# Kernel tuning notes

Measured on AMD Instinct MI355X. Metric: run time of the kernel, lower is better.

## Reference

```python
import jax, jax.numpy as jnp
import numpy as np

EPSILON = 1e-8
K = 3  # three-nearest-neighbor interpolation


def setup_inputs() -> dict:
    key = jax.random.key(0)
    k1, k2, k3 = jax.random.split(key, 3)
    B, N1, N2, C = 8, 1024, 4096, 256
    p1 = jax.random.normal(k1, (B, N1, 3), dtype=jnp.float32)  # coarse coords
    x1 = jax.random.normal(k2, (B, C, N1), dtype=jnp.float32)  # coarse features (channel-first)
    p2 = jax.random.normal(k3, (B, N2, 3), dtype=jnp.float32)  # fine coords
    return {"p1": p1, "x1": x1, "p2": p2}


def reference(p1, x1, p2):
    # Squared pairwise distances [B, N2, N1] via the expansion trick.
    d2 = (
        jnp.sum(p2 * p2, axis=-1, keepdims=True)
        - 2.0 * jnp.einsum("bmd,bnd->bmn", p2, p1)
        + jnp.sum(p1 * p1, axis=-1)[:, None, :]
    )
    # K smallest distances (pointops.nearestneighbor returns squared dists).
    neg_top, idx = jax.lax.top_k(-d2, K)  # [B, N2, K]
    dist = -neg_top
    # Reciprocal-distance weights, normalized over the K neighbors.
    dist_recip = 1.0 / (dist + EPSILON)
    weight = dist_recip / jnp.sum(dist_recip, axis=-1, keepdims=True)  # [B, N2, K]
    # Gather neighbor features and blend: up_x1[b,c,m] = sum_k w[b,m,k] * x1[b,c,idx[b,m,k]]
    x1t = jnp.swapaxes(x1, 1, 2)  # [B, N1, C]
    gathered = jax.vmap(lambda f, i: f[i])(x1t, idx)  # [B, N2, K, C]
    up_x1 = jnp.einsum("bmkc,bmk->bcm", gathered, weight)  # [B, C, N2]
    return up_x1
```

## Files before the change

kernel.cpp:

```cpp
#include <hip/hip_runtime.h>
#include <cfloat>
#include <climits>

#define B_   8
#define N1_  1024
#define N2_  4096
#define C_   256
#define TPQ  16
#define QPB  (256 / TPQ)


__device__ __forceinline__ bool better_(float d, int i, float D, int I) {
    return (d < D) || (d == D && i < I);
}

__device__ __forceinline__ void ins_(float d, int i,
                                     float& d0, float& d1, float& d2,
                                     int& i0, int& i1, int& i2) {
    if (better_(d, i, d2, i2)) {
        d2 = d; i2 = i;
        if (better_(d2, i2, d1, i1)) {
            float td = d1; d1 = d2; d2 = td;
            int   ti = i1; i1 = i2; i2 = ti;
            if (better_(d1, i1, d0, i0)) {
                td = d0; d0 = d1; d1 = td;
                ti = i0; i0 = i1; i1 = ti;
            }
        }
    }
}

__global__ __launch_bounds__(256) void knn_kernel(
    const float* __restrict__ p1, const float* __restrict__ p2,
    int4* __restrict__ wsi, float4* __restrict__ wsw) {
    __shared__ float4 pts[N1_];

    const int tid   = threadIdx.x;
    const int b     = blockIdx.x >> 8;
    const int mtile = blockIdx.x & 255;

    for (int j = tid; j < N1_; j += 256) {
        float x = p1[((size_t)b * N1_ + j) * 3 + 0];
        float y = p1[((size_t)b * N1_ + j) * 3 + 1];
        float z = p1[((size_t)b * N1_ + j) * 3 + 2];
        float s1 = __fadd_rn(__fadd_rn(__fmul_rn(x, x), __fmul_rn(y, y)),
                             __fmul_rn(z, z));
        pts[j] = make_float4(x + x, y + y, z + z, s1);
    }
    __syncthreads();

    const int q = tid >> 4;
    const int t = tid & 15;
    const int m = mtile * QPB + q;

    const size_t pbase = ((size_t)b * N2_ + m) * 3;
    const float x2 = p2[pbase + 0];
    const float y2 = p2[pbase + 1];
    const float z2 = p2[pbase + 2];
    const float s2 = __fadd_rn(__fadd_rn(__fmul_rn(x2, x2), __fmul_rn(y2, y2)),
                               __fmul_rn(z2, z2));

    float d0 = FLT_MAX, d1 = FLT_MAX, d2 = FLT_MAX;
    int   i0 = INT_MAX, i1 = INT_MAX, i2 = INT_MAX;

#pragma unroll 4
    for (int n = t; n < N1_; n += TPQ) {
        float4 p = pts[n];
        float dot2 = __fadd_rn(__fadd_rn(__fmul_rn(x2, p.x), __fmul_rn(y2, p.y)),
                               __fmul_rn(z2, p.z));
        float dd = __fadd_rn(__fsub_rn(s2, dot2), p.w);

        bool c0 = dd < d0;
        bool c1 = dd < d1;
        bool c2 = dd < d2;
        float n0 = fminf(dd, d0);
        float n1 = __builtin_amdgcn_fmed3f(dd, d0, d1);
        float n2 = __builtin_amdgcn_fmed3f(dd, d1, d2);
        int j0 = c0 ? n : i0;
        int j1 = c1 ? (c0 ? i0 : n) : i1;
        int j2 = c2 ? (c1 ? i1 : n) : i2;
        d0 = n0; d1 = n1; d2 = n2;
        i0 = j0; i1 = j1; i2 = j2;
    }

    for (int mask = 1; mask < TPQ; mask <<= 1) {
        float pd0 = __shfl_xor(d0, mask, TPQ);
        float pd1 = __shfl_xor(d1, mask, TPQ);
        float pd2 = __shfl_xor(d2, mask, TPQ);
        int   pi0 = __shfl_xor(i0, mask, TPQ);
        int   pi1 = __shfl_xor(i1, mask, TPQ);
        int   pi2 = __shfl_xor(i2, mask, TPQ);
        ins_(pd0, pi0, d0, d1, d2, i0, i1, i2);
        ins_(pd1, pi1, d0, d1, d2, i0, i1, i2);
        ins_(pd2, pi2, d0, d1, d2, i0, i1, i2);
    }

    if (t == 0) {
        float r0 = 1.0f / __fadd_rn(d0, 1e-8f);
        float r1 = 1.0f / __fadd_rn(d1, 1e-8f);
        float r2 = 1.0f / __fadd_rn(d2, 1e-8f);
        float s  = __fadd_rn(__fadd_rn(r0, r1), r2);
        const size_t o = (size_t)b * N2_ + m;
        wsi[o] = make_int4(i0, i1, i2, 0);
        wsw[o] = make_float4(r0 / s, r1 / s, r2 / s, 0.0f);
    }
}


__global__ __launch_bounds__(256) void blend_kernel(
    const float* __restrict__ x1, const int4* __restrict__ wsi,
    const float4* __restrict__ wsw, float* __restrict__ out) {
    __shared__ float4 L4[N1_];

    int bid = blockIdx.x;
    const int mhalf = bid & 1;
    const int ct    = (bid >> 1) & 63;
    const int b     = bid >> 7;
    const int tid   = threadIdx.x;

    const size_t wbase = (size_t)b * N2_ + (size_t)mhalf * 2048;
    int4   id[8];
    float4 w[8];
#pragma unroll
    for (int mb = 0; mb < 8; ++mb) {
        id[mb] = wsi[wbase + mb * 256 + tid];
        w[mb]  = wsw[wbase + mb * 256 + tid];
    }

    const float* src = x1 + ((size_t)b * C_ + (size_t)ct * 4) * N1_;
    float4 v[4];
#pragma unroll
    for (int c = 0; c < 4; ++c)
        v[c] = reinterpret_cast<const float4*>(src + (size_t)c * N1_)[tid];
#pragma unroll
    for (int e = 0; e < 4; ++e) {
        const int n = 4 * tid + e;
        L4[n ^ ((n >> 3) & 7)] = make_float4((&v[0].x)[e], (&v[1].x)[e],
                                             (&v[2].x)[e], (&v[3].x)[e]);
    }
    __syncthreads();

    const size_t obase = ((size_t)b * C_ + (size_t)ct * 4) * N2_;
#pragma unroll
    for (int mb = 0; mb < 8; ++mb) {
        const int m = mhalf * 2048 + mb * 256 + tid;
        const int na = id[mb].x, nb = id[mb].y, nc = id[mb].z;
        const float4 A  = L4[na ^ ((na >> 3) & 7)];
        const float4 Bv = L4[nb ^ ((nb >> 3) & 7)];
        const float4 Cv = L4[nc ^ ((nc >> 3) & 7)];
        const float wx = w[mb].x, wy = w[mb].y, wz = w[mb].z;
#pragma unroll
        for (int r = 0; r < 4; ++r) {
            float acc = __fadd_rn(__fadd_rn(__fmul_rn((&A.x)[r],  wx),
                                            __fmul_rn((&Bv.x)[r], wy)),
                                  __fmul_rn((&Cv.x)[r], wz));
            __builtin_nontemporal_store(acc, &out[obase + (size_t)r * N2_ + m]);
        }
    }
}

extern "C" void kernel_launch(void* const* d_in, const int* in_sizes, int n_in,
                              void* d_out, int out_size, void* d_ws, size_t ws_size,
                              hipStream_t stream) {
    const float* p1 = (const float*)d_in[0];
    const float* x1 = (const float*)d_in[1];
    const float* p2 = (const float*)d_in[2];
    float* out = (float*)d_out;

    int4*   wsi = (int4*)d_ws;
    float4* wsw = (float4*)((char*)d_ws + (size_t)B_ * N2_ * sizeof(int4));

    knn_kernel<<<B_ * (N2_ / QPB), 256, 0, stream>>>(p1, p2, wsi, wsw);
    blend_kernel<<<B_ * (C_ / 4) * 2, 256, 0, stream>>>(x1, wsi, wsw, out);
}
```

Baseline: 33.07 us.

## Pack distance and index into sortable keys, process four queries per thread

Rewrites the KNN kernel so each thread handles four queries over a 32-point slice, using packed float2 math. Each distance is truncated and packed with its 10-bit index into one unsigned key, so top-4 insertion becomes a chain of integer min/max ops. The exact top-3 is then recovered by recomputing the four candidate distances and sorting them. This cuts the per-point compare/select cost and amortizes shared-memory loads across queries, but adds register pressure and relies on four truncated candidates containing the true top three.

```diff
diff --git a/kernel.cpp b/kernel.cpp
--- a/kernel.cpp
+++ b/kernel.cpp
@@ -6,38 +6,37 @@
 #define N1_  1024
 #define N2_  4096
 #define C_   256
-#define TPQ  16
-#define QPB  (256 / TPQ)
-
-
-__device__ __forceinline__ bool better_(float d, int i, float D, int I) {
-    return (d < D) || (d == D && i < I);
-}
-
-__device__ __forceinline__ void ins_(float d, int i,
-                                     float& d0, float& d1, float& d2,
-                                     int& i0, int& i1, int& i2) {
-    if (better_(d, i, d2, i2)) {
-        d2 = d; i2 = i;
-        if (better_(d2, i2, d1, i1)) {
-            float td = d1; d1 = d2; d2 = td;
-            int   ti = i1; i1 = i2; i2 = ti;
-            if (better_(d1, i1, d0, i0)) {
-                td = d0; d0 = d1; d1 = td;
-                ti = i0; i0 = i1; i1 = ti;
-            }
-        }
-    }
-}
+#define QPT  4
+#define QPB  32
+
+typedef float vf2 __attribute__((ext_vector_type(2)));
+
+__device__ __forceinline__ unsigned umin_(unsigned a, unsigned b) { return a < b ? a : b; }
+__device__ __forceinline__ unsigned umax_(unsigned a, unsigned b) { return a > b ? a : b; }
+
+#define KINS4(k, k0, k1, k2, k3) do {                 \
+    unsigned _n1 = umax_(k0, umin_((k), k1));         \
+    unsigned _n2 = umax_(k1, umin_((k), k2));         \
+    unsigned _n3 = umax_(k2, umin_((k), k3));         \
+    k0 = umin_((k), k0);  k1 = _n1;  k2 = _n2;  k3 = _n3; \
+} while (0)
 
 __global__ __launch_bounds__(256) void knn_kernel(
     const float* __restrict__ p1, const float* __restrict__ p2,
     int4* __restrict__ wsi, float4* __restrict__ wsw) {
+#pragma clang fp contract(off)
     __shared__ float4 pts[N1_];
 
     const int tid   = threadIdx.x;
-    const int b     = blockIdx.x >> 8;
-    const int mtile = blockIdx.x & 255;
+    const int b     = blockIdx.x >> 7;
+    const int mtile = blockIdx.x & 127;
+    const int slice = tid & 31;
+    const int slot  = tid >> 5;
+    const int mbase = mtile * QPB + slot * QPT;
+
+    const float4* P4 = reinterpret_cast<const float4*>(
+        p2 + ((size_t)b * N2_ + mbase) * 3);
+    const float4 f0 = P4[0], f1 = P4[1], f2 = P4[2];
 
     for (int j = tid; j < N1_; j += 256) {
         float x = p1[((size_t)b * N1_ + j) * 3 + 0];
@@ -47,61 +46,108 @@
                              __fmul_rn(z, z));
         pts[j] = make_float4(x + x, y + y, z + z, s1);
     }
+
+    const float x0 = f0.x, y0 = f0.y, z0 = f0.z;
+    const float x1q = f0.w, y1q = f1.x, z1q = f1.y;
+    const float x2q = f1.z, y2q = f1.w, z2q = f2.x;
+    const float x3q = f2.y, y3q = f2.z, z3q = f2.w;
+    const vf2 xA = {x0, x1q}, xB = {x2q, x3q};
+    const vf2 yA = {y0, y1q}, yB = {y2q, y3q};
+    const vf2 zA = {z0, z1q}, zB = {z2q, z3q};
+    const vf2 sA = (xA * xA + yA * yA) + zA * zA;
+    const vf2 sB = (xB * xB + yB * yB) + zB * zB;
+
     __syncthreads();
 
-    const int q = tid >> 4;
-    const int t = tid & 15;
-    const int m = mtile * QPB + q;
-
-    const size_t pbase = ((size_t)b * N2_ + m) * 3;
-    const float x2 = p2[pbase + 0];
-    const float y2 = p2[pbase + 1];
-    const float z2 = p2[pbase + 2];
-    const float s2 = __fadd_rn(__fadd_rn(__fmul_rn(x2, x2), __fmul_rn(y2, y2)),
-                               __fmul_rn(z2, z2));
-
-    float d0 = FLT_MAX, d1 = FLT_MAX, d2 = FLT_MAX;
-    int   i0 = INT_MAX, i1 = INT_MAX, i2 = INT_MAX;
-
-#pragma unroll 4
-    for (int n = t; n < N1_; n += TPQ) {
-        float4 p = pts[n];
-        float dot2 = __fadd_rn(__fadd_rn(__fmul_rn(x2, p.x), __fmul_rn(y2, p.y)),
-                               __fmul_rn(z2, p.z));
-        float dd = __fadd_rn(__fsub_rn(s2, dot2), p.w);
-
-        bool c0 = dd < d0;
-        bool c1 = dd < d1;
-        bool c2 = dd < d2;
-        float n0 = fminf(dd, d0);
-        float n1 = __builtin_amdgcn_fmed3f(dd, d0, d1);
-        float n2 = __builtin_amdgcn_fmed3f(dd, d1, d2);
-        int j0 = c0 ? n : i0;
-        int j1 = c1 ? (c0 ? i0 : n) : i1;
-        int j2 = c2 ? (c1 ? i1 : n) : i2;
-        d0 = n0; d1 = n1; d2 = n2;
-        i0 = j0; i1 = j1; i2 = j2;
-    }
-
-    for (int mask = 1; mask < TPQ; mask <<= 1) {
-        float pd0 = __shfl_xor(d0, mask, TPQ);
-        float pd1 = __shfl_xor(d1, mask, TPQ);
-        float pd2 = __shfl_xor(d2, mask, TPQ);
-        int   pi0 = __shfl_xor(i0, mask, TPQ);
-        int   pi1 = __shfl_xor(i1, mask, TPQ);
-        int   pi2 = __shfl_xor(i2, mask, TPQ);
-        ins_(pd0, pi0, d0, d1, d2, i0, i1, i2);
-        ins_(pd1, pi1, d0, d1, d2, i0, i1, i2);
-        ins_(pd2, pi2, d0, d1, d2, i0, i1, i2);
-    }
-
-    if (t == 0) {
-        float r0 = 1.0f / __fadd_rn(d0, 1e-8f);
-        float r1 = 1.0f / __fadd_rn(d1, 1e-8f);
-        float r2 = 1.0f / __fadd_rn(d2, 1e-8f);
-        float s  = __fadd_rn(__fadd_rn(r0, r1), r2);
-        const size_t o = (size_t)b * N2_ + m;
-        wsi[o] = make_int4(i0, i1, i2, 0);
+    unsigned k00 = UINT_MAX, k01 = UINT_MAX, k02 = UINT_MAX, k03 = UINT_MAX;
+    unsigned k10 = UINT_MAX, k11 = UINT_MAX, k12 = UINT_MAX, k13 = UINT_MAX;
+    unsigned k20 = UINT_MAX, k21 = UINT_MAX, k22 = UINT_MAX, k23 = UINT_MAX;
+    unsigned k30 = UINT_MAX, k31 = UINT_MAX, k32 = UINT_MAX, k33 = UINT_MAX;
+
+#pragma unroll 8
+    for (int j = 0; j < N1_ / 32; ++j) {
+        const int n = j * 32 + slice;
+        const float4 c = pts[n];
+        const vf2 cx = {c.x, c.x}, cy = {c.y, c.y};
+        const vf2 cz = {c.z, c.z}, cw = {c.w, c.w};
+        const vf2 dA = (sA - ((xA * cx + yA * cy) + zA * cz)) + cw;
+        const vf2 dB = (sB - ((xB * cx + yB * cy) + zB * cz)) + cw;
+        const unsigned un = (unsigned)n;
+        const unsigned q0 = (__float_as_uint(fmaxf(dA.x, 0.f)) & 0xFFFFFC00u) | un;
+        const unsigned q1 = (__float_as_uint(fmaxf(dA.y, 0.f)) & 0xFFFFFC00u) | un;
+        const unsigned q2 = (__float_as_uint(fmaxf(dB.x, 0.f)) & 0xFFFFFC00u) | un;
+        const unsigned q3 = (__float_as_uint(fmaxf(dB.y, 0.f)) & 0xFFFFFC00u) | un;
+        KINS4(q0, k00, k01, k02, k03);
+        KINS4(q1, k10, k11, k12, k13);
+        KINS4(q2, k20, k21, k22, k23);
+        KINS4(q3, k30, k31, k32, k33);
+    }
+
+#pragma unroll
+    for (int mask = 1; mask < 32; mask <<= 1) {
+        unsigned p0, p1_, p2_, p3_;
+        p0  = (unsigned)__shfl_xor((int)k00, mask, 32);
+        p1_ = (unsigned)__shfl_xor((int)k01, mask, 32);
+        p2_ = (unsigned)__shfl_xor((int)k02, mask, 32);
+        p3_ = (unsigned)__shfl_xor((int)k03, mask, 32);
+        KINS4(p0, k00, k01, k02, k03); KINS4(p1_, k00, k01, k02, k03);
+        KINS4(p2_, k00, k01, k02, k03); KINS4(p3_, k00, k01, k02, k03);
+        p0  = (unsigned)__shfl_xor((int)k10, mask, 32);
+        p1_ = (unsigned)__shfl_xor((int)k11, mask, 32);
+        p2_ = (unsigned)__shfl_xor((int)k12, mask, 32);
+        p3_ = (unsigned)__shfl_xor((int)k13, mask, 32);
+        KINS4(p0, k10, k11, k12, k13); KINS4(p1_, k10, k11, k12, k13);
+        KINS4(p2_, k10, k11, k12, k13); KINS4(p3_, k10, k11, k12, k13);
+        p0  = (unsigned)__shfl_xor((int)k20, mask, 32);
+        p1_ = (unsigned)__shfl_xor((int)k21, mask, 32);
+        p2_ = (unsigned)__shfl_xor((int)k22, mask, 32);
+        p3_ = (unsigned)__shfl_xor((int)k23, mask, 32);
+        KINS4(p0, k20, k21, k22, k23); KINS4(p1_, k20, k21, k22, k23);
+        KINS4(p2_, k20, k21, k22, k23); KINS4(p3_, k20, k21, k22, k23);
+        p0  = (unsigned)__shfl_xor((int)k30, mask, 32);
+        p1_ = (unsigned)__shfl_xor((int)k31, mask, 32);
+        p2_ = (unsigned)__shfl_xor((int)k32, mask, 32);
+        p3_ = (unsigned)__shfl_xor((int)k33, mask, 32);
+        KINS4(p0, k30, k31, k32, k33); KINS4(p1_, k30, k31, k32, k33);
+        KINS4(p2_, k30, k31, k32, k33); KINS4(p3_, k30, k31, k32, k33);
+    }
+
+    if (slice < QPT) {
+        const unsigned a0 = slice == 0 ? k00 : slice == 1 ? k10 : slice == 2 ? k20 : k30;
+        const unsigned a1 = slice == 0 ? k01 : slice == 1 ? k11 : slice == 2 ? k21 : k31;
+        const unsigned a2 = slice == 0 ? k02 : slice == 1 ? k12 : slice == 2 ? k22 : k32;
+        const unsigned a3 = slice == 0 ? k03 : slice == 1 ? k13 : slice == 2 ? k23 : k33;
+        const float qx = slice == 0 ? x0 : slice == 1 ? x1q : slice == 2 ? x2q : x3q;
+        const float qy = slice == 0 ? y0 : slice == 1 ? y1q : slice == 2 ? y2q : y3q;
+        const float qz = slice == 0 ? z0 : slice == 1 ? z1q : slice == 2 ? z2q : z3q;
+        const float qs = slice == 0 ? sA.x : slice == 1 ? sA.y : slice == 2 ? sB.x : sB.y;
+
+        int   ix[4];
+        float dx[4];
+#pragma unroll
+        for (int k = 0; k < 4; ++k) {
+            const unsigned a = k == 0 ? a0 : k == 1 ? a1 : k == 2 ? a2 : a3;
+            const int n = (int)(a & 1023u);
+            const float4 c = pts[n];
+            dx[k] = __fadd_rn(__fsub_rn(qs,
+                __fadd_rn(__fadd_rn(__fmul_rn(qx, c.x), __fmul_rn(qy, c.y)),
+                          __fmul_rn(qz, c.z))), c.w);
+            ix[k] = n;
+        }
+#define CSWAP(a, b) do {                                            \
+        bool sw = (dx[b] < dx[a]) || (dx[b] == dx[a] && ix[b] < ix[a]); \
+        float td = sw ? dx[b] : dx[a]; dx[b] = sw ? dx[a] : dx[b]; dx[a] = td; \
+        int   ti = sw ? ix[b] : ix[a]; ix[b] = sw ? ix[a] : ix[b]; ix[a] = ti; \
+    } while (0)
+        CSWAP(0, 1); CSWAP(2, 3); CSWAP(0, 2); CSWAP(1, 3); CSWAP(1, 2);
+#undef CSWAP
+
+        const float r0 = 1.0f / __fadd_rn(dx[0], 1e-8f);
+        const float r1 = 1.0f / __fadd_rn(dx[1], 1e-8f);
+        const float r2 = 1.0f / __fadd_rn(dx[2], 1e-8f);
+        const float s  = __fadd_rn(__fadd_rn(r0, r1), r2);
+        const size_t o = (size_t)b * N2_ + mbase + slice;
+        wsi[o] = make_int4(ix[0], ix[1], ix[2], 0);
         wsw[o] = make_float4(r0 / s, r1 / s, r2 / s, 0.0f);
     }
 }
```

After: 34.94 us. 1.06x slower.

## Pack truncated distance and index into u32 keys for KNN top-k selection

Applied to the files above, without the earlier changes.

Replaces the separate float distance and int index top-3 tracking with a single 32-bit key: the distance bits with the low 10 mantissa bits replaced by the point index. A top-4 list is kept with integer med3/min, which halves the selection state and the warp shuffles. Because truncation can reorder near-ties, the four candidates are rescored exactly at the end and sorted before the top three are taken. This risks wrong neighbors only when the true third and fifth candidates fall within the truncation tolerance. Negative distances are also clamped to zero.

```diff
diff --git a/kernel.cpp b/kernel.cpp
--- a/kernel.cpp
+++ b/kernel.cpp
@@ -9,26 +9,20 @@
 #define TPQ  16
 #define QPB  (256 / TPQ)
 
+__device__ __forceinline__ unsigned umin_(unsigned a, unsigned b) { return a < b ? a : b; }
 
-__device__ __forceinline__ bool better_(float d, int i, float D, int I) {
-    return (d < D) || (d == D && i < I);
+__device__ __forceinline__ unsigned umed3_(unsigned a, unsigned b, unsigned c) {
+    unsigned d;
+    asm("v_med3_u32 %0, %1, %2, %3" : "=v"(d) : "v"(a), "v"(b), "v"(c));
+    return d;
 }
 
-__device__ __forceinline__ void ins_(float d, int i,
-                                     float& d0, float& d1, float& d2,
-                                     int& i0, int& i1, int& i2) {
-    if (better_(d, i, d2, i2)) {
-        d2 = d; i2 = i;
-        if (better_(d2, i2, d1, i1)) {
-            float td = d1; d1 = d2; d2 = td;
-            int   ti = i1; i1 = i2; i2 = ti;
-            if (better_(d1, i1, d0, i0)) {
-                td = d0; d0 = d1; d1 = td;
-                ti = i0; i0 = i1; i1 = ti;
-            }
-        }
-    }
-}
+#define KINS4(k, k0, k1, k2, k3) do {                 \
+    unsigned _n1 = umed3_((k), k0, k1);               \
+    unsigned _n2 = umed3_((k), k1, k2);               \
+    unsigned _n3 = umed3_((k), k2, k3);               \
+    k0 = umin_((k), k0);  k1 = _n1;  k2 = _n2;  k3 = _n3; \
+} while (0)
 
 __global__ __launch_bounds__(256) void knn_kernel(
     const float* __restrict__ p1, const float* __restrict__ p2,
@@ -60,8 +54,7 @@
     const float s2 = __fadd_rn(__fadd_rn(__fmul_rn(x2, x2), __fmul_rn(y2, y2)),
                                __fmul_rn(z2, z2));
 
-    float d0 = FLT_MAX, d1 = FLT_MAX, d2 = FLT_MAX;
-    int   i0 = INT_MAX, i1 = INT_MAX, i2 = INT_MAX;
+    unsigned k0 = UINT_MAX, k1 = UINT_MAX, k2 = UINT_MAX, k3 = UINT_MAX;
 
 #pragma unroll 4
     for (int n = t; n < N1_; n += TPQ) {
@@ -69,39 +62,49 @@
         float dot2 = __fadd_rn(__fadd_rn(__fmul_rn(x2, p.x), __fmul_rn(y2, p.y)),
                                __fmul_rn(z2, p.z));
         float dd = __fadd_rn(__fsub_rn(s2, dot2), p.w);
-
-        bool c0 = dd < d0;
-        bool c1 = dd < d1;
-        bool c2 = dd < d2;
-        float n0 = fminf(dd, d0);
-        float n1 = __builtin_amdgcn_fmed3f(dd, d0, d1);
-        float n2 = __builtin_amdgcn_fmed3f(dd, d1, d2);
-        int j0 = c0 ? n : i0;
-        int j1 = c1 ? (c0 ? i0 : n) : i1;
-        int j2 = c2 ? (c1 ? i1 : n) : i2;
-        d0 = n0; d1 = n1; d2 = n2;
-        i0 = j0; i1 = j1; i2 = j2;
+        unsigned key = (__float_as_uint(fmaxf(dd, 0.f)) & 0xFFFFFC00u)
+                       | (unsigned)n;
+        KINS4(key, k0, k1, k2, k3);
     }
 
     for (int mask = 1; mask < TPQ; mask <<= 1) {
-        float pd0 = __shfl_xor(d0, mask, TPQ);
-        float pd1 = __shfl_xor(d1, mask, TPQ);
-        float pd2 = __shfl_xor(d2, mask, TPQ);
-        int   pi0 = __shfl_xor(i0, mask, TPQ);
-        int   pi1 = __shfl_xor(i1, mask, TPQ);
-        int   pi2 = __shfl_xor(i2, mask, TPQ);
-        ins_(pd0, pi0, d0, d1, d2, i0, i1, i2);
-        ins_(pd1, pi1, d0, d1, d2, i0, i1, i2);
-        ins_(pd2, pi2, d0, d1, d2, i0, i1, i2);
+        unsigned p0 = (unsigned)__shfl_xor((int)k0, mask, TPQ);
+        unsigned p1_ = (unsigned)__shfl_xor((int)k1, mask, TPQ);
+        unsigned p2_ = (unsigned)__shfl_xor((int)k2, mask, TPQ);
+        unsigned p3_ = (unsigned)__shfl_xor((int)k3, mask, TPQ);
+        KINS4(p0,  k0, k1, k2, k3);
+        KINS4(p1_, k0, k1, k2, k3);
+        KINS4(p2_, k0, k1, k2, k3);
+        KINS4(p3_, k0, k1, k2, k3);
     }
 
     if (t == 0) {
-        float r0 = 1.0f / __fadd_rn(d0, 1e-8f);
-        float r1 = 1.0f / __fadd_rn(d1, 1e-8f);
-        float r2 = 1.0f / __fadd_rn(d2, 1e-8f);
-        float s  = __fadd_rn(__fadd_rn(r0, r1), r2);
+        int   ix[4];
+        float dx[4];
+#pragma unroll
+        for (int k = 0; k < 4; ++k) {
+            const unsigned a = k == 0 ? k0 : k == 1 ? k1 : k == 2 ? k2 : k3;
+            const int n = (int)(a & 1023u);
+            const float4 c = pts[n];
+            dx[k] = __fadd_rn(__fsub_rn(s2,
+                __fadd_rn(__fadd_rn(__fmul_rn(x2, c.x), __fmul_rn(y2, c.y)),
+                          __fmul_rn(z2, c.z))), c.w);
+            ix[k] = n;
+        }
+#define CSWAP(a, b) do {                                            \
+        bool sw = (dx[b] < dx[a]) || (dx[b] == dx[a] && ix[b] < ix[a]); \
+        float td = sw ? dx[b] : dx[a]; dx[b] = sw ? dx[a] : dx[b]; dx[a] = td; \
+        int   ti = sw ? ix[b] : ix[a]; ix[b] = sw ? ix[a] : ix[b]; ix[a] = ti; \
+    } while (0)
+        CSWAP(0, 1); CSWAP(2, 3); CSWAP(0, 2); CSWAP(1, 3); CSWAP(1, 2);
+#undef CSWAP
+
+        const float r0 = 1.0f / __fadd_rn(dx[0], 1e-8f);
+        const float r1 = 1.0f / __fadd_rn(dx[1], 1e-8f);
+        const float r2 = 1.0f / __fadd_rn(dx[2], 1e-8f);
+        const float s  = __fadd_rn(__fadd_rn(r0, r1), r2);
         const size_t o = (size_t)b * N2_ + m;
-        wsi[o] = make_int4(i0, i1, i2, 0);
+        wsi[o] = make_int4(ix[0], ix[1], ix[2], 0);
         wsw[o] = make_float4(r0 / s, r1 / s, r2 / s, 0.0f);
     }
 }
```

Result: faster. 32.01 us (-3.2%).
